# Performance work log

Hardware: AMD Instinct MI355X
Metric: run time of the kernel (lower is better)

The kernel has to match this reference:

```python
import jax, jax.numpy as jnp
import numpy as np

SIZE = 1024
LATENT_DIM = 256
BETA_C = 0.25
LEGACY = True


def setup_inputs() -> dict:
    key = jax.random.key(0)
    k1, k2 = jax.random.split(key)
    z = jax.random.normal(k1, (8, LATENT_DIM, 16, 16, 16), dtype=jnp.float32)
    # nn.Embedding weight initialized uniform(-1/size, 1/size)
    embedding = jax.random.uniform(
        k2, (SIZE, LATENT_DIM), minval=-1.0 / SIZE, maxval=1.0 / SIZE, dtype=jnp.float32
    )
    return {"z": z, "embedding": embedding}


def reference(z, embedding):
    sg = jax.lax.stop_gradient
    B, C, D, H, W = z.shape
    # [B, D, H, W, C]
    zp = jnp.transpose(z, (0, 2, 3, 4, 1))
    zf = zp.reshape(-1, C)  # [N, C]
    # pairwise squared distances [N, K]
    d = (
        jnp.sum(zf * zf, axis=1, keepdims=True)
        + jnp.sum(embedding * embedding, axis=1)
        - 2.0 * (zf @ embedding.T)
    )
    idx = jnp.argmin(d, axis=1)  # [N]
    # direct gather == one-hot @ embedding
    z_q = embedding[idx].reshape(zp.shape)
    if LEGACY:
        loss = jnp.mean((sg(z_q) - zp) ** 2) + BETA_C * jnp.mean((z_q - sg(zp)) ** 2)
    else:
        loss = BETA_C * jnp.mean((sg(z_q) - zp) ** 2) + jnp.mean((z_q - sg(zp)) ** 2)
    # perplexity: e_mean = mean of one-hot encodings == normalized counts
    counts = jnp.zeros((SIZE,), dtype=z.dtype).at[idx].add(1.0)
    e_mean = counts / zf.shape[0]
    perplexity = jnp.exp(-jnp.sum(e_mean * jnp.log(e_mean + 1e-10)))
    # straight-through estimator
    z_q = zp + sg(z_q - zp)
    z_q = jnp.transpose(z_q, (0, 4, 1, 2, 3))  # back to [B, C, D, H, W]
    return z_q, loss, perplexity, idx
```

## Files before the change

kernel.cpp:

```cpp
#include <hip/hip_runtime.h>
#include <cstddef>
#include <cstdint>

#define CDIM 256
#define SPAT 4096
#define KCODE 1024

#define LOSS_OFF 8388608
#define PERP_OFF 8388609
#define IDX_OFF  8388610

typedef __bf16 bf16x8 __attribute__((ext_vector_type(8)));
typedef float floatx16 __attribute__((ext_vector_type(16)));
typedef unsigned short ushort8 __attribute__((ext_vector_type(8)));

__device__ __forceinline__ unsigned short f2bf_rne(float f) {
    union { float f; uint32_t u; } c; c.f = f;
    uint32_t u = c.u;
    return (unsigned short)((u + 0x7fffu + ((u >> 16) & 1u)) >> 16);
}
__device__ __forceinline__ float bf2f(unsigned short h) {
    union { float f; uint32_t u; } c; c.u = ((uint32_t)h) << 16;
    return c.f;
}

__device__ __forceinline__ void dma16(const void* g, void* l) {
    __builtin_amdgcn_global_load_lds(
        (const __attribute__((address_space(1))) void*)g,
        (__attribute__((address_space(3))) void*)l, 16, 0, 0);
}

__global__ __launch_bounds__(256) void vq_prep(const float* __restrict__ emb,
                                               unsigned short* __restrict__ ehsw,
                                               unsigned short* __restrict__ elsw,
                                               float* __restrict__ enorm,
                                               float* __restrict__ counts,
                                               float* __restrict__ losssum) {
    int tid = threadIdx.x;
    if (blockIdx.x == 0) {
        for (int i = tid; i < KCODE; i += 256) counts[i] = 0.0f;
        if (tid == 0) losssum[0] = 0.0f;
    }
    int w = tid >> 6, lane = tid & 63;
    int k = blockIdx.x * 4 + w;
    const float* row = emb + (size_t)k * CDIM;
    float s = 0.0f;
#pragma unroll
    for (int i = 0; i < 4; ++i) {
        float v = row[lane + 64 * i];
        s = fmaf(v, v, s);
    }
#pragma unroll
    for (int m = 32; m > 0; m >>= 1) s += __shfl_xor(s, m, 64);
    if (lane == 0) enorm[k] = s;

    float4 v4 = *(const float4*)(row + lane * 4);
    unsigned short h0 = f2bf_rne(v4.x), h1 = f2bf_rne(v4.y),
                   h2 = f2bf_rne(v4.z), h3 = f2bf_rne(v4.w);
    ushort4 hv = make_ushort4(h0, h1, h2, h3);
    ushort4 lv = make_ushort4(f2bf_rne(v4.x - bf2f(h0)), f2bf_rne(v4.y - bf2f(h1)),
                              f2bf_rne(v4.z - bf2f(h2)), f2bf_rne(v4.w - bf2f(h3)));
    int kb = lane >> 1, cj = (lane & 1) * 4;
    int st = k >> 5, ks = k & 31;
    int phys = kb ^ (ks & 7);
    size_t dst = (size_t)st * 8192 + ks * 256 + phys * 8 + cj;
    *(ushort4*)(ehsw + dst) = hv;
    *(ushort4*)(elsw + dst) = lv;
}

__global__ __launch_bounds__(256, 1) void vq_main(const float* __restrict__ z,
                                                  const float* __restrict__ emb,
                                                  const unsigned short* __restrict__ ehsw,
                                                  const unsigned short* __restrict__ elsw,
                                                  const float* __restrict__ enorm,
                                                  float* __restrict__ counts,
                                                  float* __restrict__ losssum,
                                                  float* __restrict__ out) {
    __shared__ __align__(16) unsigned char lds[131072 + 4096 + 512 + 1024 + 1024 + 512];
    float* zhalf = (float*)lds;
    float* ens_s = (float*)(lds + 131072);
    float* zzs   = (float*)(lds + 135168);
    float* pb_s  = (float*)(lds + 135680);
    int*   pb_i  = (int*)(lds + 136704);
    int*   bidxs = (int*)(lds + 137728);

    const int tid = threadIdx.x;
    const int w = tid >> 6;
    const int lane = tid & 63;
    const int m_ = lane & 31;
    const int g = lane >> 5;
    const int kh = w >> 1;
    const int cw = w & 1;
    const int n0 = blockIdx.x * 128;
    const int b = n0 >> 12;
    const int sp0 = n0 & 4095;
    const float* zb = z + (size_t)b * CDIM * SPAT + sp0;

    ushort8 zh0[16], zl0[16], zh1[16], zl1[16];

    for (int h = 0; h < 2; ++h) {
        for (int i = tid; i < CDIM * 16; i += 256) {
            int c = i >> 4, seg = i & 15;
            *(float4*)&zhalf[c * 64 + seg * 4] =
                *(const float4*)(zb + (size_t)c * SPAT + h * 64 + seg * 4);
        }
        __syncthreads();
        if (cw == h) {
#pragma unroll
            for (int t = 0; t < 2; ++t) {
#pragma unroll
                for (int kc = 0; kc < 16; ++kc) {
#pragma unroll
                    for (int j = 0; j < 8; ++j) {
                        float v = zhalf[(kc * 16 + g * 8 + j) * 64 + t * 32 + m_];
                        unsigned short hb = f2bf_rne(v);
                        unsigned short lb = f2bf_rne(v - bf2f(hb));
                        if (t == 0) { zh0[kc][j] = hb; zl0[kc][j] = lb; }
                        else        { zh1[kc][j] = hb; zl1[kc][j] = lb; }
                    }
                }
            }
        } else if (kh == 0) {
            float s = 0.0f;
            for (int c = 0; c < CDIM; ++c) {
                float v = zhalf[c * 64 + lane];
                s = fmaf(v, v, s);
            }
            zzs[h * 64 + lane] = s;
        } else if (h == 0) {
            for (int i = lane; i < KCODE; i += 64) ens_s[i] = enorm[i];
        }
        __syncthreads();
    }

    const float zzv0 = zzs[cw * 64 + m_];
    const float zzv1 = zzs[cw * 64 + 32 + m_];

    float bs0 = 3.4e38f, bs1 = 3.4e38f;
    int bi0 = 0, bi1 = 0;

    const char* gsrc = (const char*)((w & 1) ? elsw : ehsw);

    {
        const char* gp = gsrc + ((size_t)(kh * 16) << 14) + (lane << 4);
        char* lp = (char*)lds + ((size_t)w << 14);
#pragma unroll
        for (int j = 0; j < 16; ++j) dma16(gp + j * 1024, lp + j * 1024);
    }

    for (int s = 0; s < 16; ++s) {
        __syncthreads();
        if (s < 15) {
            const char* gp = gsrc + ((size_t)(kh * 16 + s + 1) << 14) + (lane << 4);
            char* lp = (char*)lds + (((size_t)(s + 1) & 1) << 16) + ((size_t)w << 14);
#pragma unroll
            for (int j = 0; j < 16; ++j) dma16(gp + j * 1024, lp + j * 1024);
            __builtin_amdgcn_sched_barrier(0);
        }
        const char* EHb = (const char*)lds + (((size_t)s & 1) << 16) + ((size_t)kh << 15);
        const char* ELb = EHb + 16384;

        floatx16 a0 = {0.0f, 0.0f, 0.0f, 0.0f, 0.0f, 0.0f, 0.0f, 0.0f,
                       0.0f, 0.0f, 0.0f, 0.0f, 0.0f, 0.0f, 0.0f, 0.0f};
        floatx16 a1 = a0;
#pragma unroll
        for (int kc = 0; kc < 16; ++kc) {
            int kb0 = kc * 2 + g;
            int off = m_ * 512 + ((kb0 ^ (m_ & 7)) << 4);
            bf16x8 aeh = *(const bf16x8*)(EHb + off);
            bf16x8 ael = *(const bf16x8*)(ELb + off);
            bf16x8 bh0 = __builtin_bit_cast(bf16x8, zh0[kc]);
            bf16x8 bl0 = __builtin_bit_cast(bf16x8, zl0[kc]);
            bf16x8 bh1 = __builtin_bit_cast(bf16x8, zh1[kc]);
            bf16x8 bl1 = __builtin_bit_cast(bf16x8, zl1[kc]);
            a0 = __builtin_amdgcn_mfma_f32_32x32x16_bf16(aeh, bh0, a0, 0, 0, 0);
            a1 = __builtin_amdgcn_mfma_f32_32x32x16_bf16(aeh, bh1, a1, 0, 0, 0);
            a0 = __builtin_amdgcn_mfma_f32_32x32x16_bf16(ael, bh0, a0, 0, 0, 0);
            a1 = __builtin_amdgcn_mfma_f32_32x32x16_bf16(ael, bh1, a1, 0, 0, 0);
            a0 = __builtin_amdgcn_mfma_f32_32x32x16_bf16(aeh, bl0, a0, 0, 0, 0);
            a1 = __builtin_amdgcn_mfma_f32_32x32x16_bf16(aeh, bl1, a1, 0, 0, 0);
        }

#pragma unroll
        for (int reg = 0; reg < 16; ++reg) {
            int mm = (reg & 3) + 8 * (reg >> 2) + 4 * g;
            int code = kh * 512 + s * 32 + mm;
            float en = ens_s[code];
            float d0 = (zzv0 + en) - 2.0f * a0[reg];
            float d1 = (zzv1 + en) - 2.0f * a1[reg];
            if (d0 < bs0) { bs0 = d0; bi0 = code; }
            if (d1 < bs1) { bs1 = d1; bi1 = code; }
        }
    }

    {
        float s2 = __shfl_xor(bs0, 32, 64);
        int i2 = __shfl_xor(bi0, 32, 64);
        if (s2 < bs0 || (s2 == bs0 && i2 < bi0)) { bs0 = s2; bi0 = i2; }
        float s3 = __shfl_xor(bs1, 32, 64);
        int i3 = __shfl_xor(bi1, 32, 64);
        if (s3 < bs1 || (s3 == bs1 && i3 < bi1)) { bs1 = s3; bi1 = i3; }
    }
    __syncthreads();
    if (lane < 32) {
        pb_s[kh * 128 + cw * 64 + m_] = bs0;
        pb_s[kh * 128 + cw * 64 + 32 + m_] = bs1;
        pb_i[kh * 128 + cw * 64 + m_] = bi0;
        pb_i[kh * 128 + cw * 64 + 32 + m_] = bi1;
    }
    __syncthreads();
    if (tid < 128) {
        float s0 = pb_s[tid], s1 = pb_s[128 + tid];
        int i0 = pb_i[tid], i1 = pb_i[128 + tid];
        int ki = (s1 < s0) ? i1 : i0;
        bidxs[tid] = ki;
        out[IDX_OFF + n0 + tid] = (float)ki;
        atomicAdd(&counts[ki], 1.0f);
    }
    __syncthreads();

    float ls = 0.0f;
    float* outz = out + (size_t)b * CDIM * SPAT + sp0;
    const int col4 = tid & 31;
    const int c_0 = tid >> 5;
    int k0 = bidxs[col4 * 4 + 0];
    int k1 = bidxs[col4 * 4 + 1];
    int k2 = bidxs[col4 * 4 + 2];
    int k3 = bidxs[col4 * 4 + 3];
    const float* e0 = emb + (size_t)k0 * CDIM;
    const float* e1 = emb + (size_t)k1 * CDIM;
    const float* e2 = emb + (size_t)k2 * CDIM;
    const float* e3 = emb + (size_t)k3 * CDIM;
    for (int c = c_0; c < CDIM; c += 8) {
        float4 zp = *(const float4*)(zb + (size_t)c * SPAT + col4 * 4);
        float d0 = e0[c] - zp.x, d1 = e1[c] - zp.y,
              d2 = e2[c] - zp.z, d3 = e3[c] - zp.w;
        float4 o;
        o.x = zp.x + d0; o.y = zp.y + d1; o.z = zp.z + d2; o.w = zp.w + d3;
        ls = fmaf(d0, d0, ls); ls = fmaf(d1, d1, ls);
        ls = fmaf(d2, d2, ls); ls = fmaf(d3, d3, ls);
        *(float4*)(outz + (size_t)c * SPAT + col4 * 4) = o;
    }
#pragma unroll
    for (int m = 32; m > 0; m >>= 1) ls += __shfl_xor(ls, m, 64);
    if (lane == 0) atomicAdd(losssum, ls);
}

__global__ __launch_bounds__(256) void vq_finalize(const float* __restrict__ counts,
                                                   const float* __restrict__ losssum,
                                                   float* __restrict__ out) {
    __shared__ float red[256];
    int tid = threadIdx.x;
    float s = 0.0f;
    for (int k = tid; k < KCODE; k += 256) {
        float em = counts[k] * (1.0f / 32768.0f);
        s += em * logf(em + 1e-10f);
    }
    red[tid] = s;
    __syncthreads();
    for (int off = 128; off > 0; off >>= 1) {
        if (tid < off) red[tid] += red[tid + off];
        __syncthreads();
    }
    if (tid == 0) {
        float m = losssum[0] * (1.0f / 8388608.0f);
        out[LOSS_OFF] = m + 0.25f * m;
        out[PERP_OFF] = expf(-red[0]);
    }
}

extern "C" void kernel_launch(void* const* d_in, const int* in_sizes, int n_in,
                              void* d_out, int out_size, void* d_ws, size_t ws_size,
                              hipStream_t stream) {
    const float* z = (const float*)d_in[0];
    const float* emb = (const float*)d_in[1];
    float* out = (float*)d_out;
    unsigned short* ehsw = (unsigned short*)d_ws;
    unsigned short* elsw = ehsw + (size_t)KCODE * CDIM;
    float* enorm = (float*)(elsw + (size_t)KCODE * CDIM);
    float* counts = enorm + KCODE;
    float* losssum = counts + KCODE;

    vq_prep<<<256, 256, 0, stream>>>(emb, ehsw, elsw, enorm, counts, losssum);
    vq_main<<<256, 256, 0, stream>>>(z, emb, ehsw, elsw, enorm, counts, losssum, out);
    vq_finalize<<<1, 256, 0, stream>>>(counts, losssum, out);
}
```

Before: 173.0 us.

## Double waves per block and stage gathered codebook rows in LDS

```diff
diff --git a/kernel.cpp b/kernel.cpp
--- a/kernel.cpp
+++ b/kernel.cpp
@@ -68,7 +68,7 @@
     *(ushort4*)(elsw + dst) = lv;
 }
 
-__global__ __launch_bounds__(256, 1) void vq_main(const float* __restrict__ z,
+__global__ __launch_bounds__(512, 2) void vq_main(const float* __restrict__ z,
                                                   const float* __restrict__ emb,
                                                   const unsigned short* __restrict__ ehsw,
                                                   const unsigned short* __restrict__ elsw,
@@ -89,96 +89,91 @@
     const int lane = tid & 63;
     const int m_ = lane & 31;
     const int g = lane >> 5;
-    const int kh = w >> 1;
-    const int cw = w & 1;
+    const int kh = w >> 2;
+    const int cq = w & 3;
+    const int ch = cq & 1;
+    const int hlf = cq >> 1;
     const int n0 = blockIdx.x * 128;
     const int b = n0 >> 12;
     const int sp0 = n0 & 4095;
     const float* zb = z + (size_t)b * CDIM * SPAT + sp0;
 
-    ushort8 zh0[16], zl0[16], zh1[16], zl1[16];
+    ushort8 zh[16], zl[16];
 
     for (int h = 0; h < 2; ++h) {
-        for (int i = tid; i < CDIM * 16; i += 256) {
+        for (int i = tid; i < CDIM * 16; i += 512) {
             int c = i >> 4, seg = i & 15;
             *(float4*)&zhalf[c * 64 + seg * 4] =
                 *(const float4*)(zb + (size_t)c * SPAT + h * 64 + seg * 4);
         }
         __syncthreads();
-        if (cw == h) {
-#pragma unroll
-            for (int t = 0; t < 2; ++t) {
-#pragma unroll
-                for (int kc = 0; kc < 16; ++kc) {
-#pragma unroll
-                    for (int j = 0; j < 8; ++j) {
-                        float v = zhalf[(kc * 16 + g * 8 + j) * 64 + t * 32 + m_];
-                        unsigned short hb = f2bf_rne(v);
-                        unsigned short lb = f2bf_rne(v - bf2f(hb));
-                        if (t == 0) { zh0[kc][j] = hb; zl0[kc][j] = lb; }
-                        else        { zh1[kc][j] = hb; zl1[kc][j] = lb; }
-                    }
+        if (hlf == h) {
+#pragma unroll
+            for (int kc = 0; kc < 16; ++kc) {
+#pragma unroll
+                for (int j = 0; j < 8; ++j) {
+                    float v = zhalf[(kc * 16 + g * 8 + j) * 64 + ch * 32 + m_];
+                    unsigned short hb = f2bf_rne(v);
+                    unsigned short lb = f2bf_rne(v - bf2f(hb));
+                    zh[kc][j] = hb; zl[kc][j] = lb;
                 }
             }
-        } else if (kh == 0) {
+        } else if (w == (h == 0 ? 2 : 0)) {
             float s = 0.0f;
             for (int c = 0; c < CDIM; ++c) {
                 float v = zhalf[c * 64 + lane];
                 s = fmaf(v, v, s);
             }
             zzs[h * 64 + lane] = s;
-        } else if (h == 0) {
+        } else if (h == 0 && w == 3) {
             for (int i = lane; i < KCODE; i += 64) ens_s[i] = enorm[i];
         }
         __syncthreads();
     }
 
-    const float zzv0 = zzs[cw * 64 + m_];
-    const float zzv1 = zzs[cw * 64 + 32 + m_];
-
-    float bs0 = 3.4e38f, bs1 = 3.4e38f;
-    int bi0 = 0, bi1 = 0;
-
-    const char* gsrc = (const char*)((w & 1) ? elsw : ehsw);
+    const float zzv = zzs[cq * 32 + m_];
+
+    float bs = 3.4e38f;
+    int bi_ = 0;
+
+    const int bufid = w >> 1;
+    const int hf = w & 1;
+    const char* gsrc = (const char*)((bufid & 1) ? elsw : ehsw);
+    const int gs0 = kh * 16;
 
     {
-        const char* gp = gsrc + ((size_t)(kh * 16) << 14) + (lane << 4);
-        char* lp = (char*)lds + ((size_t)w << 14);
-#pragma unroll
-        for (int j = 0; j < 16; ++j) dma16(gp + j * 1024, lp + j * 1024);
+        const char* gp = gsrc + ((size_t)gs0 << 14) + (hf << 13) + (lane << 4);
+        char* lp = (char*)lds + ((size_t)bufid << 14) + (hf << 13);
+#pragma unroll
+        for (int j = 0; j < 8; ++j) dma16(gp + j * 1024, lp + j * 1024);
     }
 
     for (int s = 0; s < 16; ++s) {
         __syncthreads();
         if (s < 15) {
-            const char* gp = gsrc + ((size_t)(kh * 16 + s + 1) << 14) + (lane << 4);
-            char* lp = (char*)lds + (((size_t)(s + 1) & 1) << 16) + ((size_t)w << 14);
-#pragma unroll
-            for (int j = 0; j < 16; ++j) dma16(gp + j * 1024, lp + j * 1024);
+            const char* gp = gsrc + ((size_t)(gs0 + s + 1) << 14) + (hf << 13) + (lane << 4);
+            char* lp = (char*)lds + (((size_t)(s + 1) & 1) << 16) +
+                       ((size_t)bufid << 14) + (hf << 13);
+#pragma unroll
+            for (int j = 0; j < 8; ++j) dma16(gp + j * 1024, lp + j * 1024);
             __builtin_amdgcn_sched_barrier(0);
         }
         const char* EHb = (const char*)lds + (((size_t)s & 1) << 16) + ((size_t)kh << 15);
         const char* ELb = EHb + 16384;
 
-        floatx16 a0 = {0.0f, 0.0f, 0.0f, 0.0f, 0.0f, 0.0f, 0.0f, 0.0f,
-                       0.0f, 0.0f, 0.0f, 0.0f, 0.0f, 0.0f, 0.0f, 0.0f};
-        floatx16 a1 = a0;
+        floatx16 a = {0.0f, 0.0f, 0.0f, 0.0f, 0.0f, 0.0f, 0.0f, 0.0f,
+                      0.0f, 0.0f, 0.0f, 0.0f, 0.0f, 0.0f, 0.0f, 0.0f};
 #pragma unroll
         for (int kc = 0; kc < 16; ++kc) {
             int kb0 = kc * 2 + g;
             int off = m_ * 512 + ((kb0 ^ (m_ & 7)) << 4);
             bf16x8 aeh = *(const bf16x8*)(EHb + off);
             bf16x8 ael = *(const bf16x8*)(ELb + off);
-            bf16x8 bh0 = __builtin_bit_cast(bf16x8, zh0[kc]);
-            bf16x8 bl0 = __builtin_bit_cast(bf16x8, zl0[kc]);
-            bf16x8 bh1 = __builtin_bit_cast(bf16x8, zh1[kc]);
-            bf16x8 bl1 = __builtin_bit_cast(bf16x8, zl1[kc]);
-            a0 = __builtin_amdgcn_mfma_f32_32x32x16_bf16(aeh, bh0, a0, 0, 0, 0);
-            a1 = __builtin_amdgcn_mfma_f32_32x32x16_bf16(aeh, bh1, a1, 0, 0, 0);
-            a0 = __builtin_amdgcn_mfma_f32_32x32x16_bf16(ael, bh0, a0, 0, 0, 0);
-            a1 = __builtin_amdgcn_mfma_f32_32x32x16_bf16(ael, bh1, a1, 0, 0, 0);
-            a0 = __builtin_amdgcn_mfma_f32_32x32x16_bf16(aeh, bl0, a0, 0, 0, 0);
-            a1 = __builtin_amdgcn_mfma_f32_32x32x16_bf16(aeh, bl1, a1, 0, 0, 0);
+            bf16x8 bh = __builtin_bit_cast(bf16x8, zh[kc]);
+            bf16x8 bl = __builtin_bit_cast(bf16x8, zl[kc]);
+            a = __builtin_amdgcn_mfma_f32_32x32x16_bf16(aeh, bh, a, 0, 0, 0);
+            a = __builtin_amdgcn_mfma_f32_32x32x16_bf16(ael, bh, a, 0, 0, 0);
+            a = __builtin_amdgcn_mfma_f32_32x32x16_bf16(aeh, bl, a, 0, 0, 0);
         }
 
 #pragma unroll
@@ -186,27 +181,20 @@
             int mm = (reg & 3) + 8 * (reg >> 2) + 4 * g;
             int code = kh * 512 + s * 32 + mm;
             float en = ens_s[code];
-            float d0 = (zzv0 + en) - 2.0f * a0[reg];
-            float d1 = (zzv1 + en) - 2.0f * a1[reg];
-            if (d0 < bs0) { bs0 = d0; bi0 = code; }
-            if (d1 < bs1) { bs1 = d1; bi1 = code; }
+            float d = (zzv + en) - 2.0f * a[reg];
+            if (d < bs) { bs = d; bi_ = code; }
         }
     }
 
     {
-        float s2 = __shfl_xor(bs0, 32, 64);
-        int i2 = __shfl_xor(bi0, 32, 64);
-        if (s2 < bs0 || (s2 == bs0 && i2 < bi0)) { bs0 = s2; bi0 = i2; }
-        float s3 = __shfl_xor(bs1, 32, 64);
-        int i3 = __shfl_xor(bi1, 32, 64);
-        if (s3 < bs1 || (s3 == bs1 && i3 < bi1)) { bs1 = s3; bi1 = i3; }
+        float s2 = __shfl_xor(bs, 32, 64);
+        int i2 = __shfl_xor(bi_, 32, 64);
+        if (s2 < bs || (s2 == bs && i2 < bi_)) { bs = s2; bi_ = i2; }
     }
     __syncthreads();
     if (lane < 32) {
-        pb_s[kh * 128 + cw * 64 + m_] = bs0;
-        pb_s[kh * 128 + cw * 64 + 32 + m_] = bs1;
-        pb_i[kh * 128 + cw * 64 + m_] = bi0;
-        pb_i[kh * 128 + cw * 64 + 32 + m_] = bi1;
+        pb_s[kh * 128 + cq * 32 + m_] = bs;
+        pb_i[kh * 128 + cq * 32 + m_] = bi_;
     }
     __syncthreads();
     if (tid < 128) {
@@ -219,31 +207,39 @@
     }
     __syncthreads();
 
-    float ls = 0.0f;
-    float* outz = out + (size_t)b * CDIM * SPAT + sp0;
-    const int col4 = tid & 31;
-    const int c_0 = tid >> 5;
-    int k0 = bidxs[col4 * 4 + 0];
-    int k1 = bidxs[col4 * 4 + 1];
-    int k2 = bidxs[col4 * 4 + 2];
-    int k3 = bidxs[col4 * 4 + 3];
-    const float* e0 = emb + (size_t)k0 * CDIM;
-    const float* e1 = emb + (size_t)k1 * CDIM;
-    const float* e2 = emb + (size_t)k2 * CDIM;
-    const float* e3 = emb + (size_t)k3 * CDIM;
-    for (int c = c_0; c < CDIM; c += 8) {
-        float4 zp = *(const float4*)(zb + (size_t)c * SPAT + col4 * 4);
-        float d0 = e0[c] - zp.x, d1 = e1[c] - zp.y,
-              d2 = e2[c] - zp.z, d3 = e3[c] - zp.w;
-        float4 o;
-        o.x = zp.x + d0; o.y = zp.y + d1; o.z = zp.z + d2; o.w = zp.w + d3;
-        ls = fmaf(d0, d0, ls); ls = fmaf(d1, d1, ls);
-        ls = fmaf(d2, d2, ls); ls = fmaf(d3, d3, ls);
-        *(float4*)(outz + (size_t)c * SPAT + col4 * 4) = o;
-    }
-#pragma unroll
-    for (int m = 32; m > 0; m >>= 1) ls += __shfl_xor(ls, m, 64);
-    if (lane == 0) atomicAdd(losssum, ls);
+#pragma unroll
+    for (int r = 0; r < 16; ++r) {
+        int row = w * 16 + r;
+        int k = bidxs[row];
+        int slot = (row & 3) * 32 + (row >> 2);
+        dma16((const char*)emb + ((size_t)k << 10) + (lane << 4),
+              (char*)lds + (size_t)slot * 1040);
+    }
+    __syncthreads();
+
+    if (tid < 256) {
+        float ls = 0.0f;
+        float* outz = out + (size_t)b * CDIM * SPAT + sp0;
+        const int col4 = tid & 31;
+        const int c_0 = tid >> 5;
+        const float* e0 = (const float*)((const char*)lds + (size_t)(0 * 32 + col4) * 1040);
+        const float* e1 = (const float*)((const char*)lds + (size_t)(1 * 32 + col4) * 1040);
+        const float* e2 = (const float*)((const char*)lds + (size_t)(2 * 32 + col4) * 1040);
+        const float* e3 = (const float*)((const char*)lds + (size_t)(3 * 32 + col4) * 1040);
+        for (int c = c_0; c < CDIM; c += 8) {
+            float4 zp = *(const float4*)(zb + (size_t)c * SPAT + col4 * 4);
+            float d0 = e0[c] - zp.x, d1 = e1[c] - zp.y,
+                  d2 = e2[c] - zp.z, d3 = e3[c] - zp.w;
+            float4 o;
+            o.x = zp.x + d0; o.y = zp.y + d1; o.z = zp.z + d2; o.w = zp.w + d3;
+            ls = fmaf(d0, d0, ls); ls = fmaf(d1, d1, ls);
+            ls = fmaf(d2, d2, ls); ls = fmaf(d3, d3, ls);
+            *(float4*)(outz + (size_t)c * SPAT + col4 * 4) = o;
+        }
+#pragma unroll
+        for (int m = 32; m > 0; m >>= 1) ls += __shfl_xor(ls, m, 64);
+        if (lane == 0) atomicAdd(losssum, ls);
+    }
 }
 
 __global__ __launch_bounds__(256) void vq_finalize(const float* __restrict__ counts,
@@ -282,6 +278,6 @@
     float* losssum = counts + KCODE;
 
     vq_prep<<<256, 256, 0, stream>>>(emb, ehsw, elsw, enorm, counts, losssum);
-    vq_main<<<256, 256, 0, stream>>>(z, emb, ehsw, elsw, enorm, counts, losssum, out);
+    vq_main<<<256, 512, 0, stream>>>(z, emb, ehsw, elsw, enorm, counts, losssum, out);
     vq_finalize<<<1, 256, 0, stream>>>(counts, losssum, out);
 }
```

Measured after the change: 157.5 us. -9.0%, faster.
